# Performance work log

Hardware: AMD Instinct MI355X
Metric: run time of the kernel (lower is better)

The kernel has to match this reference:

```python
import jax, jax.numpy as jnp
import numpy as np

EPS = 1e-5  # BatchNorm eps
N_NODES, N_EDGES, F = 100000, 600000, 128


def setup_inputs() -> dict:
    key = jax.random.key(0)
    ks = jax.random.split(key, 16)
    inp = {
        "node_representations": jax.random.normal(ks[0], (N_NODES, F), jnp.float32),
        "edges": jax.random.randint(ks[1], (2, N_EDGES), 0, N_NODES, jnp.int64 if jax.config.jax_enable_x64 else jnp.int32),
        "edge_weights": jax.random.uniform(ks[2], (N_EDGES,), jnp.float32),
        # preprocess FFN: BatchNorm1d(F) [eval mode] + Linear(F, F) + GELU
        "pre_bn_gamma": jax.random.normal(ks[3], (F,), jnp.float32) * 0.1 + 1.0,
        "pre_bn_beta": jax.random.normal(ks[4], (F,), jnp.float32) * 0.1,
        "pre_bn_mean": jax.random.normal(ks[5], (F,), jnp.float32) * 0.1,
        "pre_bn_var": jax.random.uniform(ks[6], (F,), jnp.float32) * 0.5 + 0.5,
        "pre_w": jax.random.normal(ks[7], (F, F), jnp.float32) / np.sqrt(F),
        "pre_b": jnp.zeros((F,), jnp.float32),
        # update FFN: BatchNorm1d(2F) [eval mode] + Linear(2F, F) + GELU
        "upd_bn_gamma": jax.random.normal(ks[8], (2 * F,), jnp.float32) * 0.1 + 1.0,
        "upd_bn_beta": jax.random.normal(ks[9], (2 * F,), jnp.float32) * 0.1,
        "upd_bn_mean": jax.random.normal(ks[10], (2 * F,), jnp.float32) * 0.1,
        "upd_bn_var": jax.random.uniform(ks[11], (2 * F,), jnp.float32) * 0.5 + 0.5,
        "upd_w": jax.random.normal(ks[12], (2 * F, F), jnp.float32) / np.sqrt(2 * F),
        "upd_b": jnp.zeros((F,), jnp.float32),
    }
    return inp


def _bn_eval(x, gamma, beta, mean, var):
    return (x - mean) * (gamma / jnp.sqrt(var + EPS)) + beta


def reference(node_representations, edges, edge_weights,
              pre_bn_gamma, pre_bn_beta, pre_bn_mean, pre_bn_var, pre_w, pre_b,
              upd_bn_gamma, upd_bn_beta, upd_bn_mean, upd_bn_var, upd_w, upd_b):
    n_nodes, f = node_representations.shape
    node_idx, nbr_idx = edges[0], edges[1]
    # gather neighbour features: [E, F]
    x = node_representations[nbr_idx]
    # preprocess FFN (BN eval, dropout=identity in eval, linear, gelu)
    x = _bn_eval(x, pre_bn_gamma, pre_bn_beta, pre_bn_mean, pre_bn_var)
    x = jax.nn.gelu(x @ pre_w + pre_b, approximate=False)
    x = x * edge_weights[:, None]
    # mean aggregation (replicates torch.unique-on-expanded-indices counter = degree * F)
    agg = jax.ops.segment_sum(x, node_idx, num_segments=n_nodes)
    deg = jax.ops.segment_sum(jnp.ones_like(edge_weights), node_idx, num_segments=n_nodes)
    counter = (deg * f)[:, None]
    agg = jnp.where(counter > 0, agg / jnp.where(counter > 0, counter, 1.0), 0.0)
    # concat combine + update FFN
    emb = jnp.concatenate([node_representations, agg], axis=-1)
    emb = _bn_eval(emb, upd_bn_gamma, upd_bn_beta, upd_bn_mean, upd_bn_var)
    emb = jax.nn.gelu(emb @ upd_w + upd_b, approximate=False)
    return emb
```

## Files before the change

### kernel.cpp

```cpp
#include <hip/hip_runtime.h>
#include <math.h>

#define F 128
#define TWO_F 256
#define BN_EPS 1e-5f
#define PAD_W1 136
#define PAD_W2 264

typedef unsigned short ushort_t;
typedef unsigned char uchar_t;
typedef __attribute__((ext_vector_type(8))) short bfrag;
typedef __attribute__((ext_vector_type(4))) float ffrag;
typedef __attribute__((ext_vector_type(2))) float floatx2;

__device__ __forceinline__ float gelu_exact(float x) {
    return 0.5f * x * (1.0f + erff(x * 0.70710678118654752f));
}
__device__ __forceinline__ ushort_t f2bf(float x) {
    unsigned int u = __float_as_uint(x);
    u = (u + 0x7FFFu + ((u >> 16) & 1u)) >> 16;
    return (ushort_t)u;
}
__device__ __forceinline__ unsigned int pk2(float a, float b) {
    return (unsigned int)f2bf(a) | ((unsigned int)f2bf(b) << 16);
}

__device__ __forceinline__ void fma4_fp8(float* acc, unsigned int d, float w) {
    floatx2 lo = __builtin_amdgcn_cvt_pk_f32_fp8(d, false);
    floatx2 hi = __builtin_amdgcn_cvt_pk_f32_fp8(d, true);
    acc[0] = fmaf(w, lo.x, acc[0]);
    acc[1] = fmaf(w, lo.y, acc[1]);
    acc[2] = fmaf(w, hi.x, acc[2]);
    acc[3] = fmaf(w, hi.y, acc[3]);
}
__device__ __forceinline__ void fma16_fp8(float* acc, uint4 a, float w) {
    fma4_fp8(acc + 0,  a.x, w); fma4_fp8(acc + 4,  a.y, w);
    fma4_fp8(acc + 8,  a.z, w); fma4_fp8(acc + 12, a.w, w);
}

__device__ __forceinline__ bfrag pack8(float4 f0, float4 f1) {
    bfrag a;
    unsigned int* au = reinterpret_cast<unsigned int*>(&a);
    au[0] = pk2(f0.x, f0.y); au[1] = pk2(f0.z, f0.w);
    au[2] = pk2(f1.x, f1.y); au[3] = pk2(f1.z, f1.w);
    return a;
}

__global__ __launch_bounds__(256) void fold(
    const float* __restrict__ pre_w, const float* __restrict__ pre_b,
    const float* __restrict__ g1, const float* __restrict__ be1,
    const float* __restrict__ m1, const float* __restrict__ v1,
    const float* __restrict__ upd_w, const float* __restrict__ upd_b,
    const float* __restrict__ g2, const float* __restrict__ be2,
    const float* __restrict__ m2, const float* __restrict__ v2,
    ushort_t* __restrict__ W1T, ushort_t* __restrict__ W2T,
    float* __restrict__ b1f, float* __restrict__ b2f) {
    const int t = threadIdx.x;
    if (blockIdx.x == 0) {
        __shared__ float t1[F], t2[TWO_F];
        if (t < F) {
            float s = g1[t] * rsqrtf(v1[t] + BN_EPS);
            t1[t] = be1[t] - m1[t] * s;
        }
        {
            float s = g2[t] * rsqrtf(v2[t] + BN_EPS);
            t2[t] = be2[t] - m2[t] * s;
        }
        __syncthreads();
        if (t < F) {
            float acc = pre_b[t];
            #pragma unroll 16
            for (int k = 0; k < F; ++k) acc = fmaf(t1[k], pre_w[k * F + t], acc);
            b1f[t] = acc;
        } else {
            int j = t - F;
            float acc = upd_b[j];
            #pragma unroll 16
            for (int k = 0; k < TWO_F; ++k) acc = fmaf(t2[k], upd_w[k * F + j], acc);
            b2f[j] = acc;
        }
    } else {
        int idx = (blockIdx.x - 1) * 256 + t;
        if (idx < F * F) {
            int k = idx & (F - 1), n = idx >> 7;
            float s = g1[k] * rsqrtf(v1[k] + BN_EPS);
            W1T[idx] = f2bf(s * pre_w[k * F + n]);
        }
        {
            int k = idx & (TWO_F - 1), n = idx >> 8;
            float s = g2[k] * rsqrtf(v2[k] + BN_EPS);
            W2T[idx] = f2bf(s * upd_w[k * F + n]);
        }
    }
}

__global__ __launch_bounds__(256) void hist(
    const int* __restrict__ edges, int* __restrict__ counts,
    int* __restrict__ rankb, int nEdges) {
    const int stride = gridDim.x * 256;
    for (int i = blockIdx.x * 256 + threadIdx.x; i < nEdges; i += stride) {
        int rk = atomicAdd(&counts[edges[i]], 1);
        rankb[i] = rk;
    }
}

__global__ __launch_bounds__(1024) void scan_pass1(const int* __restrict__ counts,
                                                   int* __restrict__ offsets,
                                                   int* __restrict__ blocksums, int n) {
    __shared__ int sb[1024];
    const int t = threadIdx.x;
    int idx = blockIdx.x * 1024 + t;
    int v = (idx < n) ? counts[idx] : 0;
    sb[t] = v;
    __syncthreads();
    for (int off = 1; off < 1024; off <<= 1) {
        int x = (t >= off) ? sb[t - off] : 0;
        __syncthreads();
        sb[t] += x;
        __syncthreads();
    }
    if (idx < n) offsets[idx + 1] = sb[t];
    if (t == 1023) blocksums[blockIdx.x] = sb[t];
}

__global__ __launch_bounds__(1024) void scan_pass3(const int* __restrict__ counts,
                                                   int* __restrict__ offsets,
                                                   const int* __restrict__ blocksums,
                                                   int* __restrict__ cursor, int n) {
    __shared__ int sb[1024];
    const int t = threadIdx.x;
    sb[t] = (t < blockIdx.x) ? blocksums[t] : 0;
    __syncthreads();
    #pragma unroll
    for (int off = 512; off > 0; off >>= 1) {
        if (t < off) sb[t] += sb[t + off];
        __syncthreads();
    }
    int base = sb[0];
    int idx = blockIdx.x * 1024 + t;
    if (idx < n) {
        int incl = offsets[idx + 1] + base;
        offsets[idx + 1] = incl;
        cursor[idx] = incl - counts[idx];
    }
    if (blockIdx.x == 0 && t == 0) offsets[0] = 0;
}

__global__ __launch_bounds__(256) void gemm1_fill(
    const float* __restrict__ nodes, const ushort_t* __restrict__ W1T,
    const float* __restrict__ b1f, uchar_t* __restrict__ G8, int nNodes,
    const int* __restrict__ edges, const float* __restrict__ ew,
    const int* __restrict__ offsets, const int* __restrict__ rankb,
    int2* __restrict__ csr, int nEdges,
    int gemmBlocks, int fillBlocks, int nTiles) {
    __shared__ ushort_t Wl[F * PAD_W1];
    __shared__ float bsm[F];
    __shared__ uchar_t bounce[4][16 * F];
    const int t = threadIdx.x;

    if (blockIdx.x >= gemmBlocks) {
        int b = blockIdx.x - gemmBlocks;
        for (int e = b * 256 + t; e < nEdges; e += fillBlocks * 256) {
            int dst = edges[e];
            int pos = offsets[dst] + rankb[e];
            csr[pos] = make_int2(edges[nEdges + e], __float_as_int(ew[e]));
        }
        return;
    }

    for (int j = t; j < 2048; j += 256) {
        int feat = j >> 4, kc = j & 15;
        *reinterpret_cast<uint4*>(Wl + feat * PAD_W1 + kc * 8) =
            reinterpret_cast<const uint4*>(W1T)[j];
    }
    if (t < F) bsm[t] = b1f[t];
    __syncthreads();

    const int lane = t & 63, w = t >> 6;
    const int m = lane & 15, quad = lane >> 4;
    const int rr = lane >> 2, cc = (lane & 3) * 32;

    for (int tile = blockIdx.x; tile < nTiles; tile += gemmBlocks) {
        const int tb = tile * 64;
        int arow = tb + w * 16 + m;
        if (arow >= nNodes) arow = 0;
        const float* ap = nodes + (size_t)arow * F + quad * 8;

        bfrag a[4];
        #pragma unroll
        for (int kk = 0; kk < 4; ++kk) {
            float4 f0 = *reinterpret_cast<const float4*>(ap + kk * 32);
            float4 f1 = *reinterpret_cast<const float4*>(ap + kk * 32 + 4);
            a[kk] = pack8(f0, f1);
        }

        ffrag acc[8];
        #pragma unroll
        for (int c = 0; c < 8; ++c) acc[c] = (ffrag){0.f, 0.f, 0.f, 0.f};

        #pragma unroll
        for (int kk = 0; kk < 4; ++kk) {
            int k0 = kk * 32 + quad * 8;
            #pragma unroll
            for (int c = 0; c < 8; ++c) {
                bfrag b = *reinterpret_cast<const bfrag*>(Wl + (c * 16 + m) * PAD_W1 + k0);
                acc[c] = __builtin_amdgcn_mfma_f32_16x16x32_bf16(a[kk], b, acc[c], 0, 0, 0);
            }
        }

        #pragma unroll
        for (int c = 0; c < 8; ++c) {
            float bj = bsm[c * 16 + m];
            #pragma unroll
            for (int i = 0; i < 4; ++i) {
                float v = gelu_exact(acc[c][i] + bj);
                int pkd = __builtin_amdgcn_cvt_pk_fp8_f32(v, v, 0, false);
                bounce[w][(quad * 4 + i) * F + c * 16 + m] = (uchar_t)(pkd & 0xFF);
            }
        }
        uint4 d0 = *reinterpret_cast<const uint4*>(&bounce[w][rr * F + cc]);
        uint4 d1 = *reinterpret_cast<const uint4*>(&bounce[w][rr * F + cc + 16]);
        int gr = tb + w * 16 + rr;
        if (gr < nNodes) {
            *reinterpret_cast<uint4*>(G8 + (size_t)gr * F + cc) = d0;
            *reinterpret_cast<uint4*>(G8 + (size_t)gr * F + cc + 16) = d1;
        }
    }
}

__global__ __launch_bounds__(256) void gather_agg(
    const uchar_t* __restrict__ G8, const int* __restrict__ offsets,
    const int2* __restrict__ csr, ushort_t* __restrict__ agg, int nNodes) {
    const int t = threadIdx.x;
    const int gid = blockIdx.x * 32 + (t >> 3);
    const int q = t & 7;
    if (gid >= nNodes) return;
    const int s = offsets[gid], e = offsets[gid + 1];

    float acc[16];
    #pragma unroll
    for (int j = 0; j < 16; ++j) acc[j] = 0.f;

    int i = s;
    while (i < e) {
        int c = e - i;
        c = (c > 8) ? 8 : c;
        uint4 av[8];
        float wv[8];
        #pragma unroll
        for (int j = 0; j < 8; ++j) {
            if (j < c) {
                int2 m = csr[i + j];
                wv[j] = __int_as_float(m.y);
                av[j] = *reinterpret_cast<const uint4*>(
                    G8 + (size_t)(unsigned int)m.x * F + q * 16);
            }
        }
        #pragma unroll
        for (int j = 0; j < 8; ++j)
            if (j < c) fma16_fp8(acc, av[j], wv[j]);
        i += c;
    }

    const int deg = e - s;
    const float inv = (deg > 0) ? 1.0f / ((float)deg * (float)F) : 0.f;
    uint4 pv0, pv1;
    pv0.x = pk2(acc[0] * inv, acc[1] * inv);  pv0.y = pk2(acc[2] * inv, acc[3] * inv);
    pv0.z = pk2(acc[4] * inv, acc[5] * inv);  pv0.w = pk2(acc[6] * inv, acc[7] * inv);
    pv1.x = pk2(acc[8] * inv, acc[9] * inv);  pv1.y = pk2(acc[10] * inv, acc[11] * inv);
    pv1.z = pk2(acc[12] * inv, acc[13] * inv); pv1.w = pk2(acc[14] * inv, acc[15] * inv);
    uint4* d = reinterpret_cast<uint4*>(agg + (size_t)gid * F + q * 16);
    d[0] = pv0; d[1] = pv1;
}

__global__ __launch_bounds__(512, 4) void gemm2(
    const float* __restrict__ nodes, const ushort_t* __restrict__ agg,
    const ushort_t* __restrict__ W2T, const float* __restrict__ b2f,
    float* __restrict__ out, int nNodes) {
    __shared__ ushort_t Wl[F * PAD_W2];
    __shared__ float bsm[F];
    const int t = threadIdx.x;

    for (int j = t; j < 4096; j += 512) {
        int feat = j >> 5, kc = j & 31;
        *reinterpret_cast<uint4*>(Wl + feat * PAD_W2 + kc * 8) =
            reinterpret_cast<const uint4*>(W2T)[j];
    }
    if (t < F) bsm[t] = b2f[t];
    __syncthreads();

    const int lane = t & 63, w = t >> 6;
    const int m = lane & 15, quad = lane >> 4;
    const int tb = blockIdx.x * 256;

    int row0 = tb + w * 32 + m;
    int row1 = row0 + 16;
    int r0c = (row0 < nNodes) ? row0 : 0;
    int r1c = (row1 < nNodes) ? row1 : 0;
    const float*    p0n = nodes + (size_t)r0c * F + quad * 8;
    const float*    p1n = nodes + (size_t)r1c * F + quad * 8;
    const ushort_t* p0a = agg   + (size_t)r0c * F + quad * 8;
    const ushort_t* p1a = agg   + (size_t)r1c * F + quad * 8;

    ffrag acc0[8], acc1[8];
    #pragma unroll
    for (int c = 0; c < 8; ++c) {
        acc0[c] = (ffrag){0.f, 0.f, 0.f, 0.f};
        acc1[c] = (ffrag){0.f, 0.f, 0.f, 0.f};
    }

    #pragma unroll
    for (int kk = 0; kk < 8; ++kk) {
        int k0 = kk * 32 + quad * 8;
        bfrag a0, a1;
        if (kk < 4) {
            float4 f0 = *reinterpret_cast<const float4*>(p0n + kk * 32);
            float4 f1 = *reinterpret_cast<const float4*>(p0n + kk * 32 + 4);
            a0 = pack8(f0, f1);
            float4 g0 = *reinterpret_cast<const float4*>(p1n + kk * 32);
            float4 g1 = *reinterpret_cast<const float4*>(p1n + kk * 32 + 4);
            a1 = pack8(g0, g1);
        } else {
            a0 = *reinterpret_cast<const bfrag*>(p0a + (kk - 4) * 32);
            a1 = *reinterpret_cast<const bfrag*>(p1a + (kk - 4) * 32);
        }
        #pragma unroll
        for (int c = 0; c < 8; ++c) {
            bfrag b = *reinterpret_cast<const bfrag*>(Wl + (c * 16 + m) * PAD_W2 + k0);
            acc0[c] = __builtin_amdgcn_mfma_f32_16x16x32_bf16(a0, b, acc0[c], 0, 0, 0);
            acc1[c] = __builtin_amdgcn_mfma_f32_16x16x32_bf16(a1, b, acc1[c], 0, 0, 0);
        }
    }

    #pragma unroll
    for (int c = 0; c < 8; ++c) {
        int feat = c * 16 + m;
        float bj = bsm[feat];
        #pragma unroll
        for (int i = 0; i < 4; ++i) {
            int n0 = tb + w * 32 + quad * 4 + i;
            if (n0 < nNodes) out[(size_t)n0 * F + feat] = gelu_exact(acc0[c][i] + bj);
            int n1 = n0 + 16;
            if (n1 < nNodes) out[(size_t)n1 * F + feat] = gelu_exact(acc1[c][i] + bj);
        }
    }
}

extern "C" void kernel_launch(void* const* d_in, const int* in_sizes, int n_in,
                              void* d_out, int out_size, void* d_ws, size_t ws_size,
                              hipStream_t stream) {
    const float* nodes  = (const float*)d_in[0];
    const int*   edges  = (const int*)d_in[1];
    const float* ew     = (const float*)d_in[2];
    const float* pre_g  = (const float*)d_in[3];
    const float* pre_be = (const float*)d_in[4];
    const float* pre_m  = (const float*)d_in[5];
    const float* pre_v  = (const float*)d_in[6];
    const float* pre_w  = (const float*)d_in[7];
    const float* pre_b  = (const float*)d_in[8];
    const float* upd_g  = (const float*)d_in[9];
    const float* upd_be = (const float*)d_in[10];
    const float* upd_m  = (const float*)d_in[11];
    const float* upd_v  = (const float*)d_in[12];
    const float* upd_w  = (const float*)d_in[13];
    const float* upd_b  = (const float*)d_in[14];
    float* out = (float*)d_out;

    const int nNodes = in_sizes[0] / F;
    const int nEdges = in_sizes[2];
    const int nChunks = (nNodes + 1023) / 1024;
    const int histBlocks = 1024;
    const int gemmBlocks = 768;
    const int fillBlocks = 512;
    const int nTiles = (nNodes + 63) / 64;

    char* p = (char*)d_ws;
    int*      counts    = (int*)p;       p += (size_t)nNodes * 4;
    int*      offsets   = (int*)p;       p += (size_t)(nNodes + 4) * 4;
    int*      cursor    = (int*)p;       p += (size_t)nNodes * 4;
    int*      blocksums = (int*)p;       p += 1024 * 4;
    int2*     csr       = (int2*)p;      p += (size_t)nEdges * 8;
    float*    b1f       = (float*)p;     p += F * 4;
    float*    b2f       = (float*)p;     p += F * 4;
    ushort_t* W1T       = (ushort_t*)p;  p += F * F * 2;
    ushort_t* W2T       = (ushort_t*)p;  p += TWO_F * F * 2;
    uchar_t*  G8        = (uchar_t*)p;   p += (size_t)nNodes * F;
    ushort_t* agg       = (ushort_t*)p;  p += (size_t)nNodes * F * 2;
    int*      rankb     = (int*)p;

    hipMemsetAsync(counts, 0, (size_t)nNodes * 4, stream);

    fold<<<129, 256, 0, stream>>>(
        pre_w, pre_b, pre_g, pre_be, pre_m, pre_v,
        upd_w, upd_b, upd_g, upd_be, upd_m, upd_v,
        W1T, W2T, b1f, b2f);

    hist<<<histBlocks, 256, 0, stream>>>(edges, counts, rankb, nEdges);

    scan_pass1<<<nChunks, 1024, 0, stream>>>(counts, offsets, blocksums, nNodes);
    scan_pass3<<<nChunks, 1024, 0, stream>>>(counts, offsets, blocksums, cursor, nNodes);

    gemm1_fill<<<gemmBlocks + fillBlocks, 256, 0, stream>>>(
        nodes, W1T, b1f, G8, nNodes, edges, ew, offsets, rankb, csr, nEdges,
        gemmBlocks, fillBlocks, nTiles);

    gather_agg<<<(nNodes + 31) / 32, 256, 0, stream>>>(
        G8, offsets, csr, agg, nNodes);

    gemm2<<<(nNodes + 255) / 256, 512, 0, stream>>>(
        nodes, agg, W2T, b2f, out, nNodes);
}
```

Before: 254.4 us.

## Fuse fold with histogram and restructure GEMM1 to register-resident weight slices

Merges the weight-fold kernel and the edge-histogram kernel into one launch, saving a launch and letting the two overlap. GEMM1 now uses one block per 64-node tile. Each wave holds its 32-output-column slice of W1 in registers, which removes the shared-memory weight staging, the barrier and the LDS bounce buffer for the output. FP8 results are packed four at a time and written straight to global memory with narrower, less coalesced stores, and each block reloads its weights from global/L2.

```diff
diff --git a/kernel.cpp b/kernel.cpp
--- a/kernel.cpp
+++ b/kernel.cpp
@@ -4,7 +4,6 @@
 #define F 128
 #define TWO_F 256
 #define BN_EPS 1e-5f
-#define PAD_W1 136
 #define PAD_W2 264
 
 typedef unsigned short ushort_t;
@@ -46,7 +45,7 @@
     return a;
 }
 
-__global__ __launch_bounds__(256) void fold(
+__global__ __launch_bounds__(256) void fold_hist(
     const float* __restrict__ pre_w, const float* __restrict__ pre_b,
     const float* __restrict__ g1, const float* __restrict__ be1,
     const float* __restrict__ m1, const float* __restrict__ v1,
@@ -54,7 +53,9 @@
     const float* __restrict__ g2, const float* __restrict__ be2,
     const float* __restrict__ m2, const float* __restrict__ v2,
     ushort_t* __restrict__ W1T, ushort_t* __restrict__ W2T,
-    float* __restrict__ b1f, float* __restrict__ b2f) {
+    float* __restrict__ b1f, float* __restrict__ b2f,
+    const int* __restrict__ edges, int* __restrict__ counts,
+    int* __restrict__ rankb, int nEdges, int histBlocks) {
     const int t = threadIdx.x;
     if (blockIdx.x == 0) {
         __shared__ float t1[F], t2[TWO_F];
@@ -79,7 +80,7 @@
             for (int k = 0; k < TWO_F; ++k) acc = fmaf(t2[k], upd_w[k * F + j], acc);
             b2f[j] = acc;
         }
-    } else {
+    } else if (blockIdx.x <= 128) {
         int idx = (blockIdx.x - 1) * 256 + t;
         if (idx < F * F) {
             int k = idx & (F - 1), n = idx >> 7;
@@ -91,16 +92,12 @@
             float s = g2[k] * rsqrtf(v2[k] + BN_EPS);
             W2T[idx] = f2bf(s * upd_w[k * F + n]);
         }
-    }
-}
-
-__global__ __launch_bounds__(256) void hist(
-    const int* __restrict__ edges, int* __restrict__ counts,
-    int* __restrict__ rankb, int nEdges) {
-    const int stride = gridDim.x * 256;
-    for (int i = blockIdx.x * 256 + threadIdx.x; i < nEdges; i += stride) {
-        int rk = atomicAdd(&counts[edges[i]], 1);
-        rankb[i] = rk;
+    } else {
+        int b = blockIdx.x - 129;
+        for (int i = b * 256 + t; i < nEdges; i += histBlocks * 256) {
+            int rk = atomicAdd(&counts[edges[i]], 1);
+            rankb[i] = rk;
+        }
     }
 }
 
@@ -151,15 +148,11 @@
     const float* __restrict__ b1f, uchar_t* __restrict__ G8, int nNodes,
     const int* __restrict__ edges, const float* __restrict__ ew,
     const int* __restrict__ offsets, const int* __restrict__ rankb,
-    int2* __restrict__ csr, int nEdges,
-    int gemmBlocks, int fillBlocks, int nTiles) {
-    __shared__ ushort_t Wl[F * PAD_W1];
-    __shared__ float bsm[F];
-    __shared__ uchar_t bounce[4][16 * F];
-    const int t = threadIdx.x;
-
-    if (blockIdx.x >= gemmBlocks) {
-        int b = blockIdx.x - gemmBlocks;
+    int2* __restrict__ csr, int nEdges, int nTiles, int fillBlocks) {
+    const int t = threadIdx.x;
+
+    if (blockIdx.x >= nTiles) {
+        int b = blockIdx.x - nTiles;
         for (int e = b * 256 + t; e < nEdges; e += fillBlocks * 256) {
             int dst = edges[e];
             int pos = offsets[dst] + rankb[e];
@@ -168,62 +161,60 @@
         return;
     }
 
-    for (int j = t; j < 2048; j += 256) {
-        int feat = j >> 4, kc = j & 15;
-        *reinterpret_cast<uint4*>(Wl + feat * PAD_W1 + kc * 8) =
-            reinterpret_cast<const uint4*>(W1T)[j];
-    }
-    if (t < F) bsm[t] = b1f[t];
-    __syncthreads();
-
     const int lane = t & 63, w = t >> 6;
     const int m = lane & 15, quad = lane >> 4;
-    const int rr = lane >> 2, cc = (lane & 3) * 32;
-
-    for (int tile = blockIdx.x; tile < nTiles; tile += gemmBlocks) {
-        const int tb = tile * 64;
-        int arow = tb + w * 16 + m;
-        if (arow >= nNodes) arow = 0;
-        const float* ap = nodes + (size_t)arow * F + quad * 8;
-
-        bfrag a[4];
+    const int fw = w * 32;
+
+    bfrag wf[2][4];
+    #pragma unroll
+    for (int cb = 0; cb < 2; ++cb)
+        #pragma unroll
+        for (int kk = 0; kk < 4; ++kk)
+            wf[cb][kk] = *reinterpret_cast<const bfrag*>(
+                W1T + (size_t)(fw + cb * 16 + m) * F + kk * 32 + quad * 8);
+
+    float4 bias[2];
+    #pragma unroll
+    for (int cb = 0; cb < 2; ++cb)
+        bias[cb] = *reinterpret_cast<const float4*>(b1f + fw + cb * 16 + quad * 4);
+
+    const int tb = blockIdx.x * 64;
+
+    #pragma unroll 2
+    for (int g = 0; g < 4; ++g) {
+        const int node = tb + g * 16 + m;
+        const int sn = (node < nNodes) ? node : 0;
+        const float* np = nodes + (size_t)sn * F + quad * 8;
+
+        bfrag nf[4];
         #pragma unroll
         for (int kk = 0; kk < 4; ++kk) {
-            float4 f0 = *reinterpret_cast<const float4*>(ap + kk * 32);
-            float4 f1 = *reinterpret_cast<const float4*>(ap + kk * 32 + 4);
-            a[kk] = pack8(f0, f1);
-        }
-
-        ffrag acc[8];
-        #pragma unroll
-        for (int c = 0; c < 8; ++c) acc[c] = (ffrag){0.f, 0.f, 0.f, 0.f};
-
+            float4 f0 = *reinterpret_cast<const float4*>(np + kk * 32);
+            float4 f1 = *reinterpret_cast<const float4*>(np + kk * 32 + 4);
+            nf[kk] = pack8(f0, f1);
+        }
+
+        ffrag acc[2];
+        acc[0] = (ffrag){0.f, 0.f, 0.f, 0.f};
+        acc[1] = (ffrag){0.f, 0.f, 0.f, 0.f};
         #pragma unroll
         for (int kk = 0; kk < 4; ++kk) {
-            int k0 = kk * 32 + quad * 8;
+            acc[0] = __builtin_amdgcn_mfma_f32_16x16x32_bf16(wf[0][kk], nf[kk], acc[0], 0, 0, 0);
+            acc[1] = __builtin_amdgcn_mfma_f32_16x16x32_bf16(wf[1][kk], nf[kk], acc[1], 0, 0, 0);
+        }
+
+        if (node < nNodes) {
             #pragma unroll
-            for (int c = 0; c < 8; ++c) {
-                bfrag b = *reinterpret_cast<const bfrag*>(Wl + (c * 16 + m) * PAD_W1 + k0);
-                acc[c] = __builtin_amdgcn_mfma_f32_16x16x32_bf16(a[kk], b, acc[c], 0, 0, 0);
+            for (int cb = 0; cb < 2; ++cb) {
+                float v0 = gelu_exact(acc[cb][0] + bias[cb].x);
+                float v1 = gelu_exact(acc[cb][1] + bias[cb].y);
+                float v2 = gelu_exact(acc[cb][2] + bias[cb].z);
+                float v3 = gelu_exact(acc[cb][3] + bias[cb].w);
+                int pw = __builtin_amdgcn_cvt_pk_fp8_f32(v0, v1, 0, false);
+                pw = __builtin_amdgcn_cvt_pk_fp8_f32(v2, v3, pw, true);
+                *reinterpret_cast<unsigned int*>(
+                    G8 + (size_t)node * F + fw + cb * 16 + quad * 4) = (unsigned int)pw;
             }
-        }
-
-        #pragma unroll
-        for (int c = 0; c < 8; ++c) {
-            float bj = bsm[c * 16 + m];
-            #pragma unroll
-            for (int i = 0; i < 4; ++i) {
-                float v = gelu_exact(acc[c][i] + bj);
-                int pkd = __builtin_amdgcn_cvt_pk_fp8_f32(v, v, 0, false);
-                bounce[w][(quad * 4 + i) * F + c * 16 + m] = (uchar_t)(pkd & 0xFF);
-            }
-        }
-        uint4 d0 = *reinterpret_cast<const uint4*>(&bounce[w][rr * F + cc]);
-        uint4 d1 = *reinterpret_cast<const uint4*>(&bounce[w][rr * F + cc + 16]);
-        int gr = tb + w * 16 + rr;
-        if (gr < nNodes) {
-            *reinterpret_cast<uint4*>(G8 + (size_t)gr * F + cc) = d0;
-            *reinterpret_cast<uint4*>(G8 + (size_t)gr * F + cc + 16) = d1;
         }
     }
 }
@@ -370,7 +361,6 @@
     const int nEdges = in_sizes[2];
     const int nChunks = (nNodes + 1023) / 1024;
     const int histBlocks = 1024;
-    const int gemmBlocks = 768;
     const int fillBlocks = 512;
     const int nTiles = (nNodes + 63) / 64;
 
@@ -390,19 +380,17 @@
 
     hipMemsetAsync(counts, 0, (size_t)nNodes * 4, stream);
 
-    fold<<<129, 256, 0, stream>>>(
+    fold_hist<<<129 + histBlocks, 256, 0, stream>>>(
         pre_w, pre_b, pre_g, pre_be, pre_m, pre_v,
         upd_w, upd_b, upd_g, upd_be, upd_m, upd_v,
-        W1T, W2T, b1f, b2f);
-
-    hist<<<histBlocks, 256, 0, stream>>>(edges, counts, rankb, nEdges);
+        W1T, W2T, b1f, b2f, edges, counts, rankb, nEdges, histBlocks);
 
     scan_pass1<<<nChunks, 1024, 0, stream>>>(counts, offsets, blocksums, nNodes);
     scan_pass3<<<nChunks, 1024, 0, stream>>>(counts, offsets, blocksums, cursor, nNodes);
 
-    gemm1_fill<<<gemmBlocks + fillBlocks, 256, 0, stream>>>(
+    gemm1_fill<<<nTiles + fillBlocks, 256, 0, stream>>>(
         nodes, W1T, b1f, G8, nNodes, edges, ew, offsets, rankb, csr, nEdges,
-        gemmBlocks, fillBlocks, nTiles);
+        nTiles, fillBlocks);
 
     gather_agg<<<(nNodes + 31) / 32, 256, 0, stream>>>(
         G8, offsets, csr, agg, nNodes);
```

Result: no change. 258.2 us (+1.5%).
